# Optimization experiments

Measured on AMD Instinct MI355X. Metric: run time of the kernel, lower is better.

The kernel has to match this reference:

```python
import jax, jax.numpy as jnp
import numpy as np

N_NODES = 100000


def _gcn_norm(edge_index, num_nodes):
    """Add self-loops and compute symmetric GCN normalization coefficients.
    Returns (src, dst, norm) for the augmented edge list."""
    loop = jnp.arange(num_nodes, dtype=edge_index.dtype)
    src = jnp.concatenate([edge_index[0], loop])
    dst = jnp.concatenate([edge_index[1], loop])
    deg = jax.ops.segment_sum(jnp.ones_like(src, dtype=jnp.float32), dst,
                              num_segments=num_nodes)
    dinv = jnp.where(deg > 0, jax.lax.rsqrt(deg), 0.0)
    norm = dinv[src] * dinv[dst]  # [E + N]
    return src, dst, norm


def setup_inputs() -> dict:
    key = jax.random.key(0)
    ks = jax.random.split(key, 7)
    d = 64
    E = 1000000
    x = jax.random.normal(ks[0], (N_NODES, d), dtype=jnp.float32)
    edge_index = jax.random.randint(ks[1], (2, E), 0, N_NODES, dtype=jnp.int64)
    s = 1.0 / np.sqrt(d)
    Ws = jax.random.normal(ks[2], (3, d, d), dtype=jnp.float32) * s
    bs = jax.random.normal(ks[3], (3, d), dtype=jnp.float32) * 0.02
    W_out = jax.random.normal(ks[4], (d, d), dtype=jnp.float32) * s
    b_out = jax.random.normal(ks[5], (d,), dtype=jnp.float32) * 0.02
    return {"x": x, "edge_index": edge_index, "Ws": Ws, "bs": bs,
            "W_out": W_out, "b_out": b_out}


def reference(x, edge_index, Ws, bs, W_out, b_out):
    num_nodes = x.shape[0]
    src, dst, norm = _gcn_norm(edge_index, num_nodes)  # fixed graph -> compute once
    for i in range(Ws.shape[0]):  # small fixed layer count
        h = x @ Ws[i]                              # [N, d] linear transform
        msg = norm[:, None] * h[src]               # gather + scale  [E+N, d]
        x = jax.ops.segment_sum(msg, dst, num_segments=num_nodes) + bs[i]
        x = jax.nn.relu(x)
    return x @ W_out + b_out
```

## Files before the change

kernel.cpp:

```cpp
#include <hip/hip_runtime.h>
#include <hip/hip_bf16.h>

#define D 64
#define BSHIFT 8
#define BNODES 256
#define BCAP 4096
#define PTILE 2048

typedef __attribute__((ext_vector_type(8))) short short8;
typedef __attribute__((ext_vector_type(4))) float float4v;


__device__ __forceinline__ float bf16u_to_f32(unsigned short u) {
  union { unsigned int i; float f; } c;
  c.i = ((unsigned int)u) << 16;
  return c.f;
}

__device__ __forceinline__ unsigned short f32_to_bf16u(float f) {
  union { float f; unsigned int u; } c;
  c.f = f;
  unsigned int r = (c.u + 0x7fffu + ((c.u >> 16) & 1u)) >> 16;
  return (unsigned short)r;
}


__global__ void k_probe(const void* W, const void* ei, int* flags) {
  int lane = threadIdx.x & 63;
  const unsigned short* wb = (const unsigned short*)W;
  bool big = false;
  for (int i = lane; i < 512; i += 64) {
    float v = bf16u_to_f32(wb[i]);
    if (!(fabsf(v) < 100.f)) big = true;
  }
  int anybig = __any(big);
  const int* e32 = (const int*)ei;
  bool nz = (e32[2 * lane + 1] != 0);
  int anynz = __any(nz);
  if (threadIdx.x == 0) {
    flags[0] = anybig ? 1 : 0;
    flags[1] = anynz ? 0 : 1;
  }
}


__global__ __launch_bounds__(256) void k_prep(
    const void* __restrict__ Ws, const void* __restrict__ Wout,
    const void* __restrict__ bs, const void* __restrict__ bout,
    const int* __restrict__ flags, unsigned short* __restrict__ WT,
    float* __restrict__ biasf, int* __restrict__ bucket_cursor) {
  int f32 = flags[0];
  int gid = blockIdx.x * 256 + threadIdx.x;
  int stride = gridDim.x * 256;

  for (int i = gid; i < 512; i += stride) bucket_cursor[i] = i * BCAP;

  for (int i = gid; i < 4 * 4096; i += stride) {
    int l = i >> 12;
    int r = i & 4095;
    int k = r >> 6;
    int nn = r & 63;
    unsigned short v;
    if (l < 3) {
      v = f32 ? f32_to_bf16u(((const float*)Ws)[l * 4096 + r])
              : ((const unsigned short*)Ws)[l * 4096 + r];
    } else {
      v = f32 ? f32_to_bf16u(((const float*)Wout)[r])
              : ((const unsigned short*)Wout)[r];
    }
    WT[l * 4096 + nn * 64 + k] = v;
  }
  for (int i = gid; i < 4 * 64; i += stride) {
    int l = i >> 6;
    int j = i & 63;
    float v;
    if (l < 3)
      v = f32 ? ((const float*)bs)[l * 64 + j]
              : bf16u_to_f32(((const unsigned short*)bs)[l * 64 + j]);
    else
      v = f32 ? ((const float*)bout)[j]
              : bf16u_to_f32(((const unsigned short*)bout)[j]);
    biasf[i] = v;
  }
}


__global__ __launch_bounds__(256) void k_partition(
    const void* __restrict__ ei, const int* __restrict__ flags,
    int* __restrict__ bucket_cursor, int* __restrict__ packed, int e) {
  __shared__ int lhist[512];
  __shared__ int lbase[512];
  int tid = threadIdx.x;
  int t0 = blockIdx.x * PTILE;
  int tend = min(t0 + PTILE, e);
  if (t0 >= e) return;
  int i64 = flags[1];

  for (int b = tid; b < 512; b += 256) lhist[b] = 0;
  __syncthreads();

  if (i64) {
    const long long* dst = (const long long*)ei + e;
    for (int i = t0 + tid; i < tend; i += 256)
      atomicAdd(&lhist[((int)dst[i]) >> BSHIFT], 1);
  } else {
    const int* dst = (const int*)ei + e;
    for (int i = t0 + tid; i < tend; i += 256)
      atomicAdd(&lhist[dst[i] >> BSHIFT], 1);
  }
  __syncthreads();

  for (int b = tid; b < 512; b += 256) {
    int c = lhist[b];
    lbase[b] = c ? atomicAdd(&bucket_cursor[b], c) : 0;
    lhist[b] = 0;
  }
  __syncthreads();

  if (i64) {
    const long long* srcp = (const long long*)ei;
    const long long* dstp = srcp + e;
    for (int i = t0 + tid; i < tend; i += 256) {
      int s = (int)srcp[i];
      int d = (int)dstp[i];
      int b = d >> BSHIFT;
      int r = atomicAdd(&lhist[b], 1);
      packed[lbase[b] + r] = (s << BSHIFT) | (d & (BNODES - 1));
    }
  } else {
    const int* srcp = (const int*)ei;
    const int* dstp = srcp + e;
    for (int i = t0 + tid; i < tend; i += 256) {
      int s = srcp[i];
      int d = dstp[i];
      int b = d >> BSHIFT;
      int r = atomicAdd(&lhist[b], 1);
      packed[lbase[b] + r] = (s << BSHIFT) | (d & (BNODES - 1));
    }
  }
}

__global__ __launch_bounds__(256) void k_sort_csr(
    const int* __restrict__ packed, const int* __restrict__ bucket_cursor,
    int* __restrict__ csr, int2* __restrict__ rowrange,
    float* __restrict__ dinv, int n) {
  __shared__ int lcnt[BNODES];
  __shared__ int lofs[BNODES];
  __shared__ int sbuf[BNODES];
  int tid = threadIdx.x;
  int bucket = blockIdx.x;
  int node0 = bucket << BSHIFT;
  int nodes = min(BNODES, n - node0);
  int s0 = bucket * BCAP;
  int s1 = bucket_cursor[bucket];
  lcnt[tid] = 0;
  __syncthreads();
  for (int i = s0 + tid; i < s1; i += 256)
    atomicAdd(&lcnt[packed[i] & (BNODES - 1)], 1);
  __syncthreads();
  int v = lcnt[tid];
  sbuf[tid] = v;
  __syncthreads();
  for (int off = 1; off < BNODES; off <<= 1) {
    int tv = (tid >= off) ? sbuf[tid - off] : 0;
    __syncthreads();
    sbuf[tid] += tv;
    __syncthreads();
  }
  int excl = sbuf[tid] - v;
  lofs[tid] = excl;
  lcnt[tid] = 0;
  if (tid < nodes) {
    rowrange[node0 + tid] = make_int2(s0 + excl, s0 + excl + v);
    dinv[node0 + tid] = rsqrtf((float)(v + 1));
  }
  __syncthreads();
  for (int i = s0 + tid; i < s1; i += 256) {
    int pk = packed[i];
    int ld = pk & (BNODES - 1);
    int r = atomicAdd(&lcnt[ld], 1);
    csr[s0 + lofs[ld] + r] = pk >> BSHIFT;
  }
}


__global__ __launch_bounds__(256) void k_scale(
    const void* __restrict__ x0, const int* __restrict__ flags,
    const float* __restrict__ dinv, ushort4* __restrict__ z, int n16) {
  int f32 = flags[0];
  int i = blockIdx.x * 256 + threadIdx.x;
  int stride = gridDim.x * 256;
  for (; i < n16; i += stride) {
    float d = dinv[i >> 4];
    ushort4 o;
    if (f32) {
      float4 v = ((const float4*)x0)[i];
      o.x = f32_to_bf16u(d * v.x);
      o.y = f32_to_bf16u(d * v.y);
      o.z = f32_to_bf16u(d * v.z);
      o.w = f32_to_bf16u(d * v.w);
    } else {
      ushort4 v = ((const ushort4*)x0)[i];
      o.x = f32_to_bf16u(d * bf16u_to_f32(v.x));
      o.y = f32_to_bf16u(d * bf16u_to_f32(v.y));
      o.z = f32_to_bf16u(d * bf16u_to_f32(v.z));
      o.w = f32_to_bf16u(d * bf16u_to_f32(v.w));
    }
    z[i] = o;
  }
}

__global__ __launch_bounds__(256, 4) void k_fused(
    const unsigned short* __restrict__ z, const int2* __restrict__ rowrange,
    const int* __restrict__ csr, const float* __restrict__ dinv,
    const unsigned short* __restrict__ WT, const float* __restrict__ biasf,
    unsigned short* __restrict__ out, int n, int scale_out) {
  __shared__ unsigned short ybf[16 * 80];
  int tid = threadIdx.x;
  int lane = tid & 63;
  int w = tid >> 6;
  int q = lane >> 4;
  int f = lane & 15;

  short8 b0 = *(const short8*)(WT + (size_t)(f + 16 * w) * 64 + q * 8);
  short8 b1 = *(const short8*)(WT + (size_t)(f + 16 * w) * 64 + 32 + q * 8);

  int row0 = blockIdx.x * 16;
  int base_node = row0 + w * 4;
  const ushort4* z4 = (const ushort4*)z;

  int2 rr[4];
#pragma unroll
  for (int j = 0; j < 4; j++) rr[j] = rowrange[base_node + j];

  float ac[4][4];
#pragma unroll
  for (int j = 0; j < 4; j++) {
    ushort4 sv = z4[(size_t)(base_node + j) * 16 + f];
    ac[j][0] = (q == 0) ? bf16u_to_f32(sv.x) : 0.f;
    ac[j][1] = (q == 0) ? bf16u_to_f32(sv.y) : 0.f;
    ac[j][2] = (q == 0) ? bf16u_to_f32(sv.z) : 0.f;
    ac[j][3] = (q == 0) ? bf16u_to_f32(sv.w) : 0.f;
  }

  int srcs[16];
  bool mm[16];
#pragma unroll
  for (int j = 0; j < 4; j++) {
#pragma unroll
    for (int u = 0; u < 4; u++) {
      int i = rr[j].x + 4 * u + q;
      bool m = i < rr[j].y;
      mm[j * 4 + u] = m;
      srcs[j * 4 + u] = csr[m ? i : rr[j].x];
    }
  }
  ushort4 g[16];
#pragma unroll
  for (int t = 0; t < 16; t++) g[t] = z4[(size_t)srcs[t] * 16 + f];
#pragma unroll
  for (int j = 0; j < 4; j++) {
#pragma unroll
    for (int u = 0; u < 4; u++) {
      ushort4 v = g[j * 4 + u];
      if (mm[j * 4 + u]) {
        ac[j][0] += bf16u_to_f32(v.x);
        ac[j][1] += bf16u_to_f32(v.y);
        ac[j][2] += bf16u_to_f32(v.z);
        ac[j][3] += bf16u_to_f32(v.w);
      }
    }
  }

#pragma unroll
  for (int j = 0; j < 4; j++) {
    for (int base = rr[j].x + 16; base < rr[j].y; base += 16) {
      int ts[4];
      bool tm[4];
#pragma unroll
      for (int u = 0; u < 4; u++) {
        int i = base + 4 * u + q;
        tm[u] = i < rr[j].y;
        ts[u] = csr[tm[u] ? i : rr[j].x];
      }
      ushort4 tv[4];
#pragma unroll
      for (int u = 0; u < 4; u++) tv[u] = z4[(size_t)ts[u] * 16 + f];
#pragma unroll
      for (int u = 0; u < 4; u++) {
        if (tm[u]) {
          ac[j][0] += bf16u_to_f32(tv[u].x);
          ac[j][1] += bf16u_to_f32(tv[u].y);
          ac[j][2] += bf16u_to_f32(tv[u].z);
          ac[j][3] += bf16u_to_f32(tv[u].w);
        }
      }
    }
  }

#pragma unroll
  for (int j = 0; j < 4; j++) {
#pragma unroll
    for (int c = 0; c < 4; c++) {
      ac[j][c] += __shfl_xor(ac[j][c], 16, 64);
      ac[j][c] += __shfl_xor(ac[j][c], 32, 64);
    }
  }
  if (q == 0) {
#pragma unroll
    for (int j = 0; j < 4; j++) {
      float dv = dinv[base_node + j];
      ushort4 o;
      o.x = f32_to_bf16u(dv * ac[j][0]);
      o.y = f32_to_bf16u(dv * ac[j][1]);
      o.z = f32_to_bf16u(dv * ac[j][2]);
      o.w = f32_to_bf16u(dv * ac[j][3]);
      *(ushort4*)&ybf[(w * 4 + j) * 80 + 4 * f] = o;
    }
  }
  __syncthreads();

  short8 a0 = *(const short8*)&ybf[f * 80 + q * 8];
  short8 a1 = *(const short8*)&ybf[f * 80 + 32 + q * 8];
  float4v zz = {0.f, 0.f, 0.f, 0.f};
  float4v acc = __builtin_amdgcn_mfma_f32_16x16x32_bf16(a0, b0, zz, 0, 0, 0);
  acc = __builtin_amdgcn_mfma_f32_16x16x32_bf16(a1, b1, acc, 0, 0, 0);

  float bv = biasf[16 * w + f];
  if (scale_out) {
    float4 dv4 = *(const float4*)(dinv + row0 + q * 4);
    float d[4] = {dv4.x, dv4.y, dv4.z, dv4.w};
#pragma unroll
    for (int reg = 0; reg < 4; reg++) {
      int row = row0 + q * 4 + reg;
      if (row < n)
        out[(size_t)row * 64 + 16 * w + f] =
            f32_to_bf16u(d[reg] * fmaxf(acc[reg] + bv, 0.f));
    }
  } else {
#pragma unroll
    for (int reg = 0; reg < 4; reg++) {
      int row = row0 + q * 4 + reg;
      if (row < n)
        out[(size_t)row * 64 + 16 * w + f] =
            f32_to_bf16u(fmaxf(acc[reg] + bv, 0.f));
    }
  }
}

__global__ __launch_bounds__(256) void k_gemm_final(
    const unsigned short* __restrict__ xin,
    const unsigned short* __restrict__ WT, const float* __restrict__ bias,
    void* __restrict__ out, const int* __restrict__ flags, int ntiles) {
  int lane = threadIdx.x & 63;
  int wid = threadIdx.x >> 6;
  int f = lane & 15;
  int q = lane >> 4;

  short8 bfr[4][2];
#pragma unroll
  for (int ct = 0; ct < 4; ct++)
#pragma unroll
    for (int kt = 0; kt < 2; kt++)
      bfr[ct][kt] =
          *(const short8*)(WT + (size_t)(f + 16 * ct) * 64 + kt * 32 + q * 8);

  int wave = blockIdx.x * 4 + wid;
  int nwaves = gridDim.x * 4;
  for (int t = wave; t < ntiles; t += nwaves) {
    int row0 = t * 16;
    const unsigned short* xr = xin + (size_t)(row0 + f) * 64 + q * 8;
    short8 a0 = *(const short8*)(xr);
    short8 a1 = *(const short8*)(xr + 32);
    float4v acc[4];
#pragma unroll
    for (int ct = 0; ct < 4; ct++) {
      float4v z = {0.f, 0.f, 0.f, 0.f};
      acc[ct] =
          __builtin_amdgcn_mfma_f32_16x16x32_bf16(a0, bfr[ct][0], z, 0, 0, 0);
      acc[ct] = __builtin_amdgcn_mfma_f32_16x16x32_bf16(a1, bfr[ct][1],
                                                        acc[ct], 0, 0, 0);
    }
    int f32o = flags[0];
    float bv[4];
#pragma unroll
    for (int ct = 0; ct < 4; ct++) bv[ct] = bias[f + 16 * ct];
    if (f32o) {
      float* op = (float*)out;
#pragma unroll
      for (int reg = 0; reg < 4; reg++) {
        size_t rb = (size_t)(row0 + q * 4 + reg) * 64 + f;
#pragma unroll
        for (int ct = 0; ct < 4; ct++) op[rb + 16 * ct] = acc[ct][reg] + bv[ct];
      }
    } else {
      unsigned short* op = (unsigned short*)out;
#pragma unroll
      for (int reg = 0; reg < 4; reg++) {
        size_t rb = (size_t)(row0 + q * 4 + reg) * 64 + f;
#pragma unroll
        for (int ct = 0; ct < 4; ct++)
          op[rb + 16 * ct] = f32_to_bf16u(acc[ct][reg] + bv[ct]);
      }
    }
  }
}


extern "C" void kernel_launch(void* const* d_in, const int* in_sizes, int n_in,
                              void* d_out, int out_size, void* d_ws,
                              size_t ws_size, hipStream_t stream) {
  const void* x0 = d_in[0];
  const void* ei = d_in[1];
  const void* Ws = d_in[2];
  const void* bs = d_in[3];
  const void* Wout = d_in[4];
  const void* bout = d_in[5];

  const int N = in_sizes[0] / D;
  const int E = in_sizes[1] / 2;
  const int NBUC = (N + BNODES - 1) >> BSHIFT;
  const int NT = (N + 15) / 16;

  char* p = (char*)d_ws;
  auto alloc = [&](size_t bytes) {
    char* r = p;
    p += (bytes + 511) & ~(size_t)511;
    return r;
  };
  int* flags = (int*)alloc(8);
  int* bucket_cursor = (int*)alloc(512 * 4);
  int* packed = (int*)alloc((size_t)512 * BCAP * 4);
  int* csr = (int*)alloc((size_t)512 * BCAP * 4);
  int2* rowrange = (int2*)alloc((size_t)N * 8);
  float* dinv = (float*)alloc((size_t)N * 4);
  unsigned short* WT = (unsigned short*)alloc(4 * 4096 * 2);
  float* biasf = (float*)alloc(4 * 64 * 4);
  unsigned short* za = (unsigned short*)alloc((size_t)N * D * 2);
  unsigned short* zb = (unsigned short*)alloc((size_t)N * D * 2);
  (void)ws_size;
  (void)n_in;
  (void)out_size;

  k_probe<<<1, 64, 0, stream>>>(Ws, ei, flags);
  k_prep<<<32, 256, 0, stream>>>(Ws, Wout, bs, bout, flags, WT, biasf,
                                 bucket_cursor);
  int ptiles = (E + PTILE - 1) / PTILE;
  k_partition<<<ptiles, 256, 0, stream>>>(ei, flags, bucket_cursor, packed, E);
  k_sort_csr<<<NBUC, 256, 0, stream>>>(packed, bucket_cursor, csr, rowrange,
                                       dinv, N);
  k_scale<<<1024, 256, 0, stream>>>(x0, flags, dinv, (ushort4*)za, N * 16);

  k_fused<<<NT, 256, 0, stream>>>(za, rowrange, csr, dinv, WT + 0 * 4096,
                                  biasf + 0 * 64, zb, N, 1);
  k_fused<<<NT, 256, 0, stream>>>(zb, rowrange, csr, dinv, WT + 1 * 4096,
                                  biasf + 1 * 64, za, N, 1);
  k_fused<<<NT, 256, 0, stream>>>(za, rowrange, csr, dinv, WT + 2 * 4096,
                                  biasf + 2 * 64, zb, N, 0);
  k_gemm_final<<<(NT + 3) / 4, 256, 0, stream>>>(zb, WT + 3 * 4096,
                                                 biasf + 3 * 64, d_out, flags,
                                                 NT);
}
```

Measured before the change: 265.4 us.

## Split aggregation into feature-sliced gather kernel plus separate MFMA GEMM

```diff
diff --git a/kernel.cpp b/kernel.cpp
--- a/kernel.cpp
+++ b/kernel.cpp
@@ -184,166 +184,188 @@
 }
 
 
-__global__ __launch_bounds__(256) void k_scale(
+__global__ __launch_bounds__(256) void k_scale_sliced(
     const void* __restrict__ x0, const int* __restrict__ flags,
-    const float* __restrict__ dinv, ushort4* __restrict__ z, int n16) {
+    const float* __restrict__ dinv, unsigned short* __restrict__ zs, int n,
+    int nr) {
+  __shared__ unsigned short xt[256 * 76];
+  int tid = threadIdx.x;
+  int node0 = blockIdx.x * 256;
   int f32 = flags[0];
-  int i = blockIdx.x * 256 + threadIdx.x;
-  int stride = gridDim.x * 256;
-  for (; i < n16; i += stride) {
-    float d = dinv[i >> 4];
-    ushort4 o;
-    if (f32) {
-      float4 v = ((const float4*)x0)[i];
-      o.x = f32_to_bf16u(d * v.x);
-      o.y = f32_to_bf16u(d * v.y);
-      o.z = f32_to_bf16u(d * v.z);
-      o.w = f32_to_bf16u(d * v.w);
+
+  if (f32) {
+    const float* xf = (const float*)x0;
+    for (int idx = tid; idx < 256 * 16; idx += 256) {
+      int nl = idx >> 4;
+      int c = idx & 15;
+      if (node0 + nl < n) {
+        float4 v = *(const float4*)(xf + (size_t)(node0 + nl) * 64 + c * 4);
+        ushort4 o;
+        o.x = f32_to_bf16u(v.x);
+        o.y = f32_to_bf16u(v.y);
+        o.z = f32_to_bf16u(v.z);
+        o.w = f32_to_bf16u(v.w);
+        *(ushort4*)&xt[nl * 76 + c * 4] = o;
+      }
+    }
+  } else {
+    const unsigned short* xb = (const unsigned short*)x0;
+    for (int idx = tid; idx < 256 * 8; idx += 256) {
+      int nl = idx >> 3;
+      int c = idx & 7;
+      if (node0 + nl < n) {
+        short8 v = *(const short8*)(xb + (size_t)(node0 + nl) * 64 + c * 8);
+        *(short8*)&xt[nl * 76 + c * 8] = v;
+      }
+    }
+  }
+  __syncthreads();
+
+  for (int u = tid; u < 2048; u += 256) {
+    int slice = u >> 9;
+    int rem = u & 511;
+    int nl = rem >> 1;
+    int h = rem & 1;
+    int node = node0 + nl;
+    if (node < n) {
+      float dv = dinv[node];
+      const unsigned short* src = &xt[nl * 76 + slice * 16 + h * 8];
+      unsigned short o[8];
+#pragma unroll
+      for (int k = 0; k < 8; k++) o[k] = f32_to_bf16u(dv * bf16u_to_f32(src[k]));
+      short8 ov;
+#pragma unroll
+      for (int k = 0; k < 8; k++) ov[k] = (short)o[k];
+      *(short8*)(zs + (size_t)slice * nr * 16 + (size_t)node * 16 + h * 8) = ov;
+    }
+  }
+}
+
+__global__ __launch_bounds__(256) void k_agg_sliced(
+    const unsigned short* __restrict__ zs, const int2* __restrict__ rowrange,
+    const int* __restrict__ csr, const float* __restrict__ dinv,
+    unsigned short* __restrict__ ys, int n, int nr) {
+  int slot = blockIdx.x & 7;
+  int chunk = blockIdx.x >> 3;
+  int slice = slot & 3;
+  int half = slot >> 2;
+  int node = chunk * 512 + half * 256 + threadIdx.x;
+  if (node >= n) return;
+
+  const unsigned short* zb = zs + (size_t)slice * nr * 16;
+  int2 rr = rowrange[node];
+  float dv = dinv[node];
+
+  float acc[16];
+  {
+    short8 s0 = *(const short8*)(zb + (size_t)node * 16);
+    short8 s1 = *(const short8*)(zb + (size_t)node * 16 + 8);
+#pragma unroll
+    for (int k = 0; k < 8; k++) {
+      acc[k] = bf16u_to_f32((unsigned short)s0[k]);
+      acc[8 + k] = bf16u_to_f32((unsigned short)s1[k]);
+    }
+  }
+
+  int i = rr.x;
+  for (; i + 1 < rr.y; i += 2) {
+    int sa = csr[i];
+    int sb = csr[i + 1];
+    short8 a0 = *(const short8*)(zb + (size_t)sa * 16);
+    short8 a1 = *(const short8*)(zb + (size_t)sa * 16 + 8);
+    short8 b0 = *(const short8*)(zb + (size_t)sb * 16);
+    short8 b1 = *(const short8*)(zb + (size_t)sb * 16 + 8);
+#pragma unroll
+    for (int k = 0; k < 8; k++) {
+      acc[k] += bf16u_to_f32((unsigned short)a0[k]);
+      acc[8 + k] += bf16u_to_f32((unsigned short)a1[k]);
+      acc[k] += bf16u_to_f32((unsigned short)b0[k]);
+      acc[8 + k] += bf16u_to_f32((unsigned short)b1[k]);
+    }
+  }
+  if (i < rr.y) {
+    int sa = csr[i];
+    short8 a0 = *(const short8*)(zb + (size_t)sa * 16);
+    short8 a1 = *(const short8*)(zb + (size_t)sa * 16 + 8);
+#pragma unroll
+    for (int k = 0; k < 8; k++) {
+      acc[k] += bf16u_to_f32((unsigned short)a0[k]);
+      acc[8 + k] += bf16u_to_f32((unsigned short)a1[k]);
+    }
+  }
+
+  short8 o0, o1;
+#pragma unroll
+  for (int k = 0; k < 8; k++) {
+    o0[k] = (short)f32_to_bf16u(dv * acc[k]);
+    o1[k] = (short)f32_to_bf16u(dv * acc[8 + k]);
+  }
+  unsigned short* yb = ys + (size_t)slice * nr * 16 + (size_t)node * 16;
+  *(short8*)(yb) = o0;
+  *(short8*)(yb + 8) = o1;
+}
+
+__global__ __launch_bounds__(256) void k_gemm_mid(
+    const unsigned short* __restrict__ ys,
+    const unsigned short* __restrict__ WT, const float* __restrict__ bias,
+    const float* __restrict__ dinv, unsigned short* __restrict__ out,
+    int ntiles, int nr, int scale_out) {
+  int lane = threadIdx.x & 63;
+  int wid = threadIdx.x >> 6;
+  int f = lane & 15;
+  int q = lane >> 4;
+
+  short8 bfr[4][2];
+#pragma unroll
+  for (int ct = 0; ct < 4; ct++)
+#pragma unroll
+    for (int kt = 0; kt < 2; kt++)
+      bfr[ct][kt] =
+          *(const short8*)(WT + (size_t)(f + 16 * ct) * 64 + kt * 32 + q * 8);
+
+  float bv[4];
+#pragma unroll
+  for (int ct = 0; ct < 4; ct++) bv[ct] = bias[f + 16 * ct];
+
+  size_t slice_stride = (size_t)nr * 16;
+  int wave = blockIdx.x * 4 + wid;
+  int nwaves = gridDim.x * 4;
+  for (int t = wave; t < ntiles; t += nwaves) {
+    int row0 = t * 16;
+    const unsigned short* ar =
+        ys + (size_t)(q >> 1) * slice_stride + (size_t)(row0 + f) * 16 +
+        (q & 1) * 8;
+    short8 a0 = *(const short8*)(ar);
+    short8 a1 = *(const short8*)(ar + 2 * slice_stride);
+    float4v acc[4];
+#pragma unroll
+    for (int ct = 0; ct < 4; ct++) {
+      float4v z = {0.f, 0.f, 0.f, 0.f};
+      acc[ct] =
+          __builtin_amdgcn_mfma_f32_16x16x32_bf16(a0, bfr[ct][0], z, 0, 0, 0);
+      acc[ct] = __builtin_amdgcn_mfma_f32_16x16x32_bf16(a1, bfr[ct][1],
+                                                        acc[ct], 0, 0, 0);
+    }
+    if (scale_out) {
+      float4 dv4 = *(const float4*)(dinv + row0 + q * 4);
+      float d[4] = {dv4.x, dv4.y, dv4.z, dv4.w};
+#pragma unroll
+      for (int reg = 0; reg < 4; reg++) {
+        int row = row0 + q * 4 + reg;
+#pragma unroll
+        for (int ct = 0; ct < 4; ct++)
+          out[(size_t)ct * slice_stride + (size_t)row * 16 + f] =
+              f32_to_bf16u(d[reg] * fmaxf(acc[ct][reg] + bv[ct], 0.f));
+      }
     } else {
-      ushort4 v = ((const ushort4*)x0)[i];
-      o.x = f32_to_bf16u(d * bf16u_to_f32(v.x));
-      o.y = f32_to_bf16u(d * bf16u_to_f32(v.y));
-      o.z = f32_to_bf16u(d * bf16u_to_f32(v.z));
-      o.w = f32_to_bf16u(d * bf16u_to_f32(v.w));
-    }
-    z[i] = o;
-  }
-}
-
-__global__ __launch_bounds__(256, 4) void k_fused(
-    const unsigned short* __restrict__ z, const int2* __restrict__ rowrange,
-    const int* __restrict__ csr, const float* __restrict__ dinv,
-    const unsigned short* __restrict__ WT, const float* __restrict__ biasf,
-    unsigned short* __restrict__ out, int n, int scale_out) {
-  __shared__ unsigned short ybf[16 * 80];
-  int tid = threadIdx.x;
-  int lane = tid & 63;
-  int w = tid >> 6;
-  int q = lane >> 4;
-  int f = lane & 15;
-
-  short8 b0 = *(const short8*)(WT + (size_t)(f + 16 * w) * 64 + q * 8);
-  short8 b1 = *(const short8*)(WT + (size_t)(f + 16 * w) * 64 + 32 + q * 8);
-
-  int row0 = blockIdx.x * 16;
-  int base_node = row0 + w * 4;
-  const ushort4* z4 = (const ushort4*)z;
-
-  int2 rr[4];
-#pragma unroll
-  for (int j = 0; j < 4; j++) rr[j] = rowrange[base_node + j];
-
-  float ac[4][4];
-#pragma unroll
-  for (int j = 0; j < 4; j++) {
-    ushort4 sv = z4[(size_t)(base_node + j) * 16 + f];
-    ac[j][0] = (q == 0) ? bf16u_to_f32(sv.x) : 0.f;
-    ac[j][1] = (q == 0) ? bf16u_to_f32(sv.y) : 0.f;
-    ac[j][2] = (q == 0) ? bf16u_to_f32(sv.z) : 0.f;
-    ac[j][3] = (q == 0) ? bf16u_to_f32(sv.w) : 0.f;
-  }
-
-  int srcs[16];
-  bool mm[16];
-#pragma unroll
-  for (int j = 0; j < 4; j++) {
-#pragma unroll
-    for (int u = 0; u < 4; u++) {
-      int i = rr[j].x + 4 * u + q;
-      bool m = i < rr[j].y;
-      mm[j * 4 + u] = m;
-      srcs[j * 4 + u] = csr[m ? i : rr[j].x];
-    }
-  }
-  ushort4 g[16];
-#pragma unroll
-  for (int t = 0; t < 16; t++) g[t] = z4[(size_t)srcs[t] * 16 + f];
-#pragma unroll
-  for (int j = 0; j < 4; j++) {
-#pragma unroll
-    for (int u = 0; u < 4; u++) {
-      ushort4 v = g[j * 4 + u];
-      if (mm[j * 4 + u]) {
-        ac[j][0] += bf16u_to_f32(v.x);
-        ac[j][1] += bf16u_to_f32(v.y);
-        ac[j][2] += bf16u_to_f32(v.z);
-        ac[j][3] += bf16u_to_f32(v.w);
-      }
-    }
-  }
-
-#pragma unroll
-  for (int j = 0; j < 4; j++) {
-    for (int base = rr[j].x + 16; base < rr[j].y; base += 16) {
-      int ts[4];
-      bool tm[4];
-#pragma unroll
-      for (int u = 0; u < 4; u++) {
-        int i = base + 4 * u + q;
-        tm[u] = i < rr[j].y;
-        ts[u] = csr[tm[u] ? i : rr[j].x];
-      }
-      ushort4 tv[4];
-#pragma unroll
-      for (int u = 0; u < 4; u++) tv[u] = z4[(size_t)ts[u] * 16 + f];
-#pragma unroll
-      for (int u = 0; u < 4; u++) {
-        if (tm[u]) {
-          ac[j][0] += bf16u_to_f32(tv[u].x);
-          ac[j][1] += bf16u_to_f32(tv[u].y);
-          ac[j][2] += bf16u_to_f32(tv[u].z);
-          ac[j][3] += bf16u_to_f32(tv[u].w);
-        }
-      }
-    }
-  }
-
-#pragma unroll
-  for (int j = 0; j < 4; j++) {
-#pragma unroll
-    for (int c = 0; c < 4; c++) {
-      ac[j][c] += __shfl_xor(ac[j][c], 16, 64);
-      ac[j][c] += __shfl_xor(ac[j][c], 32, 64);
-    }
-  }
-  if (q == 0) {
-#pragma unroll
-    for (int j = 0; j < 4; j++) {
-      float dv = dinv[base_node + j];
-      ushort4 o;
-      o.x = f32_to_bf16u(dv * ac[j][0]);
-      o.y = f32_to_bf16u(dv * ac[j][1]);
-      o.z = f32_to_bf16u(dv * ac[j][2]);
-      o.w = f32_to_bf16u(dv * ac[j][3]);
-      *(ushort4*)&ybf[(w * 4 + j) * 80 + 4 * f] = o;
-    }
-  }
-  __syncthreads();
-
-  short8 a0 = *(const short8*)&ybf[f * 80 + q * 8];
-  short8 a1 = *(const short8*)&ybf[f * 80 + 32 + q * 8];
-  float4v zz = {0.f, 0.f, 0.f, 0.f};
-  float4v acc = __builtin_amdgcn_mfma_f32_16x16x32_bf16(a0, b0, zz, 0, 0, 0);
-  acc = __builtin_amdgcn_mfma_f32_16x16x32_bf16(a1, b1, acc, 0, 0, 0);
-
-  float bv = biasf[16 * w + f];
-  if (scale_out) {
-    float4 dv4 = *(const float4*)(dinv + row0 + q * 4);
-    float d[4] = {dv4.x, dv4.y, dv4.z, dv4.w};
-#pragma unroll
-    for (int reg = 0; reg < 4; reg++) {
-      int row = row0 + q * 4 + reg;
-      if (row < n)
-        out[(size_t)row * 64 + 16 * w + f] =
-            f32_to_bf16u(d[reg] * fmaxf(acc[reg] + bv, 0.f));
-    }
-  } else {
-#pragma unroll
-    for (int reg = 0; reg < 4; reg++) {
-      int row = row0 + q * 4 + reg;
-      if (row < n)
-        out[(size_t)row * 64 + 16 * w + f] =
-            f32_to_bf16u(fmaxf(acc[reg] + bv, 0.f));
+#pragma unroll
+      for (int reg = 0; reg < 4; reg++) {
+        int row = row0 + q * 4 + reg;
+#pragma unroll
+        for (int ct = 0; ct < 4; ct++)
+          out[(size_t)row * 64 + 16 * ct + f] =
+              f32_to_bf16u(fmaxf(acc[ct][reg] + bv[ct], 0.f));
+      }
     }
   }
 }
@@ -421,6 +443,8 @@
   const int E = in_sizes[1] / 2;
   const int NBUC = (N + BNODES - 1) >> BSHIFT;
   const int NT = (N + 15) / 16;
+  const int NR = ((N + 511) / 512) * 512;
+  const int NCH = NR / 512;
 
   char* p = (char*)d_ws;
   auto alloc = [&](size_t bytes) {
@@ -436,8 +460,10 @@
   float* dinv = (float*)alloc((size_t)N * 4);
   unsigned short* WT = (unsigned short*)alloc(4 * 4096 * 2);
   float* biasf = (float*)alloc(4 * 64 * 4);
-  unsigned short* za = (unsigned short*)alloc((size_t)N * D * 2);
-  unsigned short* zb = (unsigned short*)alloc((size_t)N * D * 2);
+  unsigned short* za = (unsigned short*)alloc((size_t)NR * D * 2);
+  unsigned short* zb = (unsigned short*)alloc((size_t)NR * D * 2);
+  unsigned short* yy = (unsigned short*)alloc((size_t)NR * D * 2);
+  unsigned short* x3 = (unsigned short*)alloc((size_t)N * D * 2);
   (void)ws_size;
   (void)n_in;
   (void)out_size;
@@ -449,15 +475,22 @@
   k_partition<<<ptiles, 256, 0, stream>>>(ei, flags, bucket_cursor, packed, E);
   k_sort_csr<<<NBUC, 256, 0, stream>>>(packed, bucket_cursor, csr, rowrange,
                                        dinv, N);
-  k_scale<<<1024, 256, 0, stream>>>(x0, flags, dinv, (ushort4*)za, N * 16);
-
-  k_fused<<<NT, 256, 0, stream>>>(za, rowrange, csr, dinv, WT + 0 * 4096,
-                                  biasf + 0 * 64, zb, N, 1);
-  k_fused<<<NT, 256, 0, stream>>>(zb, rowrange, csr, dinv, WT + 1 * 4096,
-                                  biasf + 1 * 64, za, N, 1);
-  k_fused<<<NT, 256, 0, stream>>>(za, rowrange, csr, dinv, WT + 2 * 4096,
-                                  biasf + 2 * 64, zb, N, 0);
-  k_gemm_final<<<(NT + 3) / 4, 256, 0, stream>>>(zb, WT + 3 * 4096,
+  k_scale_sliced<<<(N + 255) / 256, 256, 0, stream>>>(x0, flags, dinv, za, N,
+                                                      NR);
+
+  k_agg_sliced<<<8 * NCH, 256, 0, stream>>>(za, rowrange, csr, dinv, yy, N, NR);
+  k_gemm_mid<<<(NT + 3) / 4, 256, 0, stream>>>(yy, WT + 0 * 4096,
+                                               biasf + 0 * 64, dinv, zb, NT,
+                                               NR, 1);
+  k_agg_sliced<<<8 * NCH, 256, 0, stream>>>(zb, rowrange, csr, dinv, yy, N, NR);
+  k_gemm_mid<<<(NT + 3) / 4, 256, 0, stream>>>(yy, WT + 1 * 4096,
+                                               biasf + 1 * 64, dinv, za, NT,
+                                               NR, 1);
+  k_agg_sliced<<<8 * NCH, 256, 0, stream>>>(za, rowrange, csr, dinv, yy, N, NR);
+  k_gemm_mid<<<(NT + 3) / 4, 256, 0, stream>>>(yy, WT + 2 * 4096,
+                                               biasf + 2 * 64, dinv, x3, NT,
+                                               NR, 0);
+  k_gemm_final<<<(NT + 3) / 4, 256, 0, stream>>>(x3, WT + 3 * 4096,
                                                  biasf + 3 * 64, d_out, flags,
                                                  NT);
 }
```

New measurement: 302.1 us. 13.8% more time.
